# Performance work log

Hardware: AMD Instinct MI355X
Metric: run time of the kernel (lower is better)

Reference implementation:

```python
import jax, jax.numpy as jnp
import numpy as np

HEADS = 8
MAX_REL = 256
D_MODEL = 512
FFN_DIM = 2048
LN_EPS = 1e-3  # keras LayerNormalization default
NEG_INF = -1e9


def _layer_norm(x, gamma, beta):
    mu = jnp.mean(x, axis=-1, keepdims=True)
    var = jnp.var(x, axis=-1, keepdims=True)
    return (x - mu) * jax.lax.rsqrt(var + LN_EPS) * gamma + beta


def _mhra(q_in, k_in, v_in, mask, p):
    """Multi-head relative-position (Shaw-style) attention.
    mask: (B, Lq, Lk), 1.0 = masked position (added as -1e9).
    """
    B, Lq, D = q_in.shape
    Lk = k_in.shape[1]
    H = HEADS
    depth = D // H
    q = (q_in @ p['Wq'] + p['bq']).reshape(B, Lq, H, depth).transpose(0, 2, 1, 3)
    k = (k_in @ p['Wk'] + p['bk']).reshape(B, Lk, H, depth).transpose(0, 2, 1, 3)
    v = (v_in @ p['Wv'] + p['bv']).reshape(B, Lk, H, depth).transpose(0, 2, 1, 3)
    # content logits (B,H,Lq,Lk)
    logits = jnp.einsum('bhqd,bhkd->bhqk', q, k)
    # relative-position logits: project q onto clipped relative embeddings
    rel_q = jnp.einsum('bhqd,rd->bhqr', q, p['rel_emb'])  # (B,H,Lq,2K+1)
    rel_idx = jnp.clip(jnp.arange(Lk)[None, :] - jnp.arange(Lq)[:, None],
                       -MAX_REL, MAX_REL) + MAX_REL  # (Lq,Lk)
    rel_logits = jnp.take_along_axis(
        rel_q, jnp.broadcast_to(rel_idx[None, None], (B, H, Lq, Lk)), axis=-1)
    scores = (logits + rel_logits) / jnp.sqrt(jnp.asarray(depth, q.dtype))
    scores = scores + mask[:, None, :, :] * NEG_INF
    weights = jax.nn.softmax(scores, axis=-1)
    out = jnp.einsum('bhqk,bhkd->bhqd', weights, v)
    out = out.transpose(0, 2, 1, 3).reshape(B, Lq, D)
    out = out @ p['Wo'] + p['bo']
    return out, weights


def _make_attn_params(key, prefix):
    ks = jax.random.split(key, 5)
    s = 0.02
    return {
        prefix + 'Wq': jax.random.normal(ks[0], (D_MODEL, D_MODEL), jnp.float32) * s,
        prefix + 'bq': jnp.zeros((D_MODEL,), jnp.float32),
        prefix + 'Wk': jax.random.normal(ks[1], (D_MODEL, D_MODEL), jnp.float32) * s,
        prefix + 'bk': jnp.zeros((D_MODEL,), jnp.float32),
        prefix + 'Wv': jax.random.normal(ks[2], (D_MODEL, D_MODEL), jnp.float32) * s,
        prefix + 'bv': jnp.zeros((D_MODEL,), jnp.float32),
        prefix + 'Wo': jax.random.normal(ks[3], (D_MODEL, D_MODEL), jnp.float32) * s,
        prefix + 'bo': jnp.zeros((D_MODEL,), jnp.float32),
        prefix + 'rel_emb': jax.random.normal(ks[4], (2 * MAX_REL + 1, D_MODEL // HEADS), jnp.float32) * s,
        prefix + 'ln_g': jnp.ones((D_MODEL,), jnp.float32),
        prefix + 'ln_b': jnp.zeros((D_MODEL,), jnp.float32),
    }


def setup_inputs() -> dict:
    key = jax.random.key(0)
    ks = jax.random.split(key, 8)
    B, Lq, Lk = 8, 1024, 1024
    inputs = jax.random.normal(ks[0], (B, Lq, D_MODEL), jnp.float32)
    enc_kv = jax.random.normal(ks[1], (B, Lk, D_MODEL), jnp.float32)
    padding_mask = jnp.zeros((B, Lq, Lk), jnp.float32)  # no encoder padding
    causal = (jnp.arange(Lk)[None, :] > jnp.arange(Lq)[:, None]).astype(jnp.float32)
    lookahead_mask = jnp.broadcast_to(causal[None], (B, Lq, Lq)).astype(jnp.float32)
    d = {'inputs': inputs, 'enc_kv': enc_kv,
         'padding_mask': padding_mask, 'lookahead_mask': lookahead_mask,
         'training': 0}
    d.update(_make_attn_params(ks[2], 'sa_'))
    d.update(_make_attn_params(ks[3], 'ca_'))
    s = 0.02
    d['ffn_W1'] = jax.random.normal(ks[4], (D_MODEL, FFN_DIM), jnp.float32) * s
    d['ffn_b1'] = jnp.zeros((FFN_DIM,), jnp.float32)
    d['ffn_W2'] = jax.random.normal(ks[5], (FFN_DIM, D_MODEL), jnp.float32) * s
    d['ffn_b2'] = jnp.zeros((D_MODEL,), jnp.float32)
    d['ffn_ln_g'] = jnp.ones((D_MODEL,), jnp.float32)
    d['ffn_ln_b'] = jnp.zeros((D_MODEL,), jnp.float32)
    return d


def reference(inputs, enc_kv, padding_mask, lookahead_mask, training,
              sa_Wq, sa_bq, sa_Wk, sa_bk, sa_Wv, sa_bv, sa_Wo, sa_bo,
              sa_rel_emb, sa_ln_g, sa_ln_b,
              ca_Wq, ca_bq, ca_Wk, ca_bk, ca_Wv, ca_bv, ca_Wo, ca_bo,
              ca_rel_emb, ca_ln_g, ca_ln_b,
              ffn_W1, ffn_b1, ffn_W2, ffn_b2, ffn_ln_g, ffn_ln_b):
    sa = {'Wq': sa_Wq, 'bq': sa_bq, 'Wk': sa_Wk, 'bk': sa_bk,
          'Wv': sa_Wv, 'bv': sa_bv, 'Wo': sa_Wo, 'bo': sa_bo,
          'rel_emb': sa_rel_emb}
    ca = {'Wq': ca_Wq, 'bq': ca_bq, 'Wk': ca_Wk, 'bk': ca_bk,
          'Wv': ca_Wv, 'bv': ca_bv, 'Wo': ca_Wo, 'bo': ca_bo,
          'rel_emb': ca_rel_emb}
    # self attention + residual + norm (dropout identity at inference)
    attn_out, attn_w = _mhra(inputs, inputs, inputs, lookahead_mask, sa)
    attn_out = _layer_norm(inputs + attn_out, sa_ln_g, sa_ln_b)
    # cross attention + residual + norm
    ca_out, ca_w = _mhra(attn_out, enc_kv, enc_kv, padding_mask, ca)
    ca_out = _layer_norm(attn_out + ca_out, ca_ln_g, ca_ln_b)
    # pointwise FFN + residual + norm
    h = jax.nn.relu(ca_out @ ffn_W1 + ffn_b1) @ ffn_W2 + ffn_b2
    out = _layer_norm(h + ca_out, ffn_ln_g, ffn_ln_b)
    return out, attn_w, ca_w
```

## Files before the change

kernel.cpp:

```cpp
#include <hip/hip_runtime.h>
#include <hip/hip_bf16.h>
#include <cstdio>


typedef __attribute__((ext_vector_type(8))) short short8v;
typedef __attribute__((ext_vector_type(4))) short short4v;
typedef __attribute__((ext_vector_type(4))) float f32x4;

static __device__ __forceinline__ unsigned short f2bf(float f) {
    unsigned int u = __float_as_uint(f);
    unsigned int r = (u + 0x7fffu + ((u >> 16) & 1u)) >> 16;
    return (unsigned short)r;
}
static __device__ __forceinline__ float bf2f(unsigned short s) {
    return __uint_as_float(((unsigned int)s) << 16);
}

static __device__ __forceinline__ f32x4 mfma_bf16(short8v a, short8v b, f32x4 c) {
    return __builtin_amdgcn_mfma_f32_16x16x32_bf16(a, b, c, 0, 0, 0);
}

static __device__ __forceinline__ void async16(const void* g, void* l) {
    __builtin_amdgcn_global_load_lds(
        (const __attribute__((address_space(1))) unsigned int*)g,
        (__attribute__((address_space(3))) unsigned int*)l,
        16, 0, 0);
}

static __device__ __forceinline__ int swz8(int bid, int nwg) {
    return (bid & 7) * (nwg >> 3) + (bid >> 3);
}


static __device__ __forceinline__ void gemm_core(
    unsigned short* As, unsigned short* Bs,
    const unsigned short* __restrict__ A, int lda,
    const unsigned short* __restrict__ BT, int ldb,
    const float* __restrict__ bias, float* __restrict__ Cf,
    unsigned short* __restrict__ Cb, int ldc,
    int m0, int n0, int Kblk, int relu)
{
    const int t = threadIdx.x, lane = t & 63, w = t >> 6;
    const int wm = w >> 1, wn = w & 1;
    const int g = lane >> 4, l15 = lane & 15;
    f32x4 acc[4][4];
#pragma unroll
    for (int m = 0; m < 4; ++m)
#pragma unroll
        for (int n = 0; n < 4; ++n) acc[m][n] = (f32x4){0.f, 0.f, 0.f, 0.f};

    const int sgl8 = (lane & 7) ^ ((lane >> 3) & 7);
    for (int k0 = 0; k0 < Kblk; k0 += 64) {
#pragma unroll
        for (int i = 0; i < 4; ++i) {
            int rbase = w * 32 + i * 8;
            async16(A  + (size_t)(m0 + rbase + (lane >> 3)) * lda + k0 + sgl8 * 8,
                    As + rbase * 64);
            async16(BT + (size_t)(n0 + rbase + (lane >> 3)) * ldb + k0 + sgl8 * 8,
                    Bs + rbase * 64);
        }
        __syncthreads();
#pragma unroll
        for (int kk = 0; kk < 2; ++kk) {
            short8v a[4], b[4];
#pragma unroll
            for (int m = 0; m < 4; ++m) {
                int row = wm * 64 + m * 16 + l15;
                a[m] = *(const short8v*)&As[row * 64 + (((kk * 4 + g) ^ (row & 7))) * 8];
            }
#pragma unroll
            for (int n = 0; n < 4; ++n) {
                int row = wn * 64 + n * 16 + l15;
                b[n] = *(const short8v*)&Bs[row * 64 + (((kk * 4 + g) ^ (row & 7))) * 8];
            }
#pragma unroll
            for (int m = 0; m < 4; ++m)
#pragma unroll
                for (int n = 0; n < 4; ++n)
                    acc[m][n] = mfma_bf16(a[m], b[n], acc[m][n]);
        }
        __syncthreads();
    }
#pragma unroll
    for (int m = 0; m < 4; ++m) {
        int gm = m0 + wm * 64 + m * 16 + (lane >> 4) * 4;
#pragma unroll
        for (int n = 0; n < 4; ++n) {
            int gn = n0 + wn * 64 + n * 16 + (lane & 15);
            float bv = bias ? bias[gn] : 0.f;
#pragma unroll
            for (int j = 0; j < 4; ++j) {
                float v = acc[m][n][j] + bv;
                if (relu) v = fmaxf(v, 0.f);
                size_t off = (size_t)(gm + j) * ldc + gn;
                if (Cf) Cf[off] = v;
                if (Cb) Cb[off] = f2bf(v);
            }
        }
    }
}

__global__ __launch_bounds__(256) void gemm_std(
    const unsigned short* __restrict__ A, int lda,
    const unsigned short* __restrict__ BT, int ldb,
    const float* __restrict__ bias,
    float* __restrict__ Cf, unsigned short* __restrict__ Cb,
    int N, int Kblk, int relu)
{
    __shared__ __attribute__((aligned(16))) unsigned short As[128 * 64];
    __shared__ __attribute__((aligned(16))) unsigned short Bs[128 * 64];
    const int kz = blockIdx.z;
    const int nwg = gridDim.x * gridDim.y;
    const int s = swz8(blockIdx.x + gridDim.x * blockIdx.y, nwg);
    const int bx = s % gridDim.x, by = s / gridDim.x;
    const size_t part = (size_t)kz * gridDim.y * 128 * N;
    gemm_core(As, Bs, A + kz * Kblk, lda, BT + kz * Kblk, ldb,
              kz == 0 ? bias : nullptr,
              Cf ? Cf + part : nullptr, Cb, N,
              by * 128, bx * 128, Kblk, relu);
}

__global__ __launch_bounds__(256) void gemm_ca(
    const unsigned short* __restrict__ Ekv, const unsigned short* __restrict__ Xq,
    const unsigned short* __restrict__ WkvT, const unsigned short* __restrict__ WqT,
    const float* __restrict__ bkv, const float* __restrict__ bq,
    unsigned short* __restrict__ KV, unsigned short* __restrict__ Q)
{
    __shared__ __attribute__((aligned(16))) unsigned short As[128 * 64];
    __shared__ __attribute__((aligned(16))) unsigned short Bs[128 * 64];
    const int nwg = gridDim.x * gridDim.y;
    const int s = swz8(blockIdx.x + gridDim.x * blockIdx.y, nwg);
    const int bx = s % gridDim.x, by = s / gridDim.x;
    if (bx < 8)
        gemm_core(As, Bs, Ekv, 512, WkvT, 512, bkv, nullptr, KV, 1024,
                  by * 128, bx * 128, 512, 0);
    else
        gemm_core(As, Bs, Xq, 512, WqT, 512, bq, nullptr, Q, 512,
                  by * 128, (bx - 8) * 128, 512, 0);
}

__global__ __launch_bounds__(256, 3) void fused_attn(
    const unsigned short* __restrict__ Qp, int qstride,
    const unsigned short* __restrict__ Kp, int kstride,
    const unsigned short* __restrict__ Vt,
    const unsigned short* __restrict__ relW,
    const unsigned short* __restrict__ maskb,
    float* __restrict__ Wout,
    unsigned short* __restrict__ Hout)
{
    __shared__ __attribute__((aligned(16))) unsigned short Qs[16 * 64];
    __shared__ __attribute__((aligned(16))) unsigned short U[24576];
    __shared__ float Red[2][4][16];
    unsigned short* Ks  = U;
    unsigned short* Rel = U;
    unsigned short* Pl  = U;
    unsigned short* Vs  = U + 16384;
    const int t = threadIdx.x, lane = t & 63, w = t >> 6;
    const int g = lane >> 4, l15 = lane & 15;
    const int s = swz8(blockIdx.x + gridDim.x * blockIdx.y, 4096);
    const int bh = s >> 6, b = bh >> 3, h = bh & 7;
    const int q0 = (s & 63) * 16;
    const int sgl8 = (lane & 7) ^ ((lane >> 3) & 7);

    if (w < 2) {
        int row = w * 8 + (lane >> 3);
        async16(Qp + (size_t)(b * 1024 + q0 + row) * qstride + h * 64 + sgl8 * 8,
                &Qs[w * 512]);
    }
    __syncthreads();

    short8v qa[2];
#pragma unroll
    for (int kk = 0; kk < 2; ++kk)
        qa[kk] = *(const short8v*)&Qs[l15 * 64 + (((kk * 4 + g) ^ (l15 & 7))) * 8];

    f32x4 acc[16];
#pragma unroll
    for (int i = 0; i < 16; ++i) acc[i] = (f32x4){0.f, 0.f, 0.f, 0.f};

#pragma unroll
    for (int qtr = 0; qtr < 4; ++qtr) {
#pragma unroll
        for (int c = 0; c < 8; ++c) {
            int rbase = w * 64 + c * 8;
            async16(Kp + (size_t)(b * 1024 + qtr * 256 + rbase + (lane >> 3)) * kstride
                       + h * 64 + sgl8 * 8,
                    &Ks[rbase * 64]);
        }
        __syncthreads();
#pragma unroll
        for (int n = 0; n < 4; ++n) {
            int row = w * 64 + n * 16 + l15;
            short8v kb0 = *(const short8v*)&Ks[row * 64 + ((g ^ (row & 7))) * 8];
            short8v kb1 = *(const short8v*)&Ks[row * 64 + (((4 + g) ^ (row & 7))) * 8];
            acc[qtr * 4 + n] = mfma_bf16(qa[0], kb0, acc[qtr * 4 + n]);
            acc[qtr * 4 + n] = mfma_bf16(qa[1], kb1, acc[qtr * 4 + n]);
        }
        __syncthreads();
    }

    for (int rs = w; rs < 33; rs += 4) {
        int rc = rs * 16 + l15;
        int re = rc > 512 ? 512 : rc;
        short8v b0 = *(const short8v*)(relW + (size_t)re * 64 + g * 8);
        short8v b1 = *(const short8v*)(relW + (size_t)re * 64 + 32 + g * 8);
        f32x4 r4 = (f32x4){0.f, 0.f, 0.f, 0.f};
        r4 = mfma_bf16(qa[0], b0, r4);
        r4 = mfma_bf16(qa[1], b1, r4);
#pragma unroll
        for (int j = 0; j < 4; ++j)
            Rel[(g * 4 + j) * 528 + rs * 16 + l15] = f2bf(r4[j]);
    }
    __syncthreads();

    const int qb = q0 + g * 4;
    const int ql = g * 4;
    const unsigned short* mrow = maskb + ((size_t)b * 1024 + qb) * 1024;
#pragma unroll
    for (int na = 0; na < 16; ++na) {
        int k = (na >> 2) * 256 + w * 64 + (na & 3) * 16 + l15;
#pragma unroll
        for (int j = 0; j < 4; ++j) {
            int q = qb + j;
            int d = k - q; d = d < -256 ? -256 : (d > 256 ? 256 : d);
            float rel = bf2f(Rel[(ql + j) * 528 + d + 256]);
            float mv = bf2f(mrow[(size_t)j * 1024 + k]);
            acc[na][j] = (acc[na][j] + rel) * 0.125f + mv;
        }
    }

    float mx[4];
#pragma unroll
    for (int j = 0; j < 4; ++j) {
        float m = acc[0][j];
#pragma unroll
        for (int na = 1; na < 16; ++na) m = fmaxf(m, acc[na][j]);
#pragma unroll
        for (int off = 1; off < 16; off <<= 1) m = fmaxf(m, __shfl_xor(m, off));
        mx[j] = m;
    }
    if (l15 == 0) {
#pragma unroll
        for (int j = 0; j < 4; ++j) Red[0][w][ql + j] = mx[j];
    }
    __syncthreads();
#pragma unroll
    for (int j = 0; j < 4; ++j) {
        float m = Red[0][0][ql + j];
        m = fmaxf(m, Red[0][1][ql + j]);
        m = fmaxf(m, Red[0][2][ql + j]);
        m = fmaxf(m, Red[0][3][ql + j]);
        mx[j] = m;
    }

    float sm[4] = {0.f, 0.f, 0.f, 0.f};
#pragma unroll
    for (int na = 0; na < 16; ++na)
#pragma unroll
        for (int j = 0; j < 4; ++j) {
            float e = __expf(acc[na][j] - mx[j]);
            acc[na][j] = e;
            sm[j] += e;
        }
#pragma unroll
    for (int j = 0; j < 4; ++j)
#pragma unroll
        for (int off = 1; off < 16; off <<= 1) sm[j] += __shfl_xor(sm[j], off);
    if (l15 == 0) {
#pragma unroll
        for (int j = 0; j < 4; ++j) Red[1][w][ql + j] = sm[j];
    }
    __syncthreads();
#pragma unroll
    for (int j = 0; j < 4; ++j) {
        float ssum = Red[1][0][ql + j] + Red[1][1][ql + j]
                   + Red[1][2][ql + j] + Red[1][3][ql + j];
        sm[j] = 1.0f / ssum;
    }

    float* wbase = Wout + ((size_t)bh * 1024 + qb) * 1024;
#pragma unroll
    for (int na = 0; na < 16; ++na) {
        int k = (na >> 2) * 256 + w * 64 + (na & 3) * 16 + l15;
#pragma unroll
        for (int j = 0; j < 4; ++j) {
            float p = acc[na][j] * sm[j];
            __builtin_nontemporal_store(p, &wbase[(size_t)j * 1024 + k]);
            Pl[((k >> 3) * 16 + (ql + j)) * 8 + (k & 7)] = f2bf(p);
        }
    }
    __syncthreads();

    f32x4 oacc = (f32x4){0.f, 0.f, 0.f, 0.f};
#pragma unroll
    for (int c = 0; c < 8; ++c) {
        {
            int idx = w * 4;
#pragma unroll
            for (int i = 0; i < 4; ++i) {
                int d = (idx + i) * 4 + (lane >> 4);
                int gl = (lane & 15) ^ (d & 15);
                async16(Vt + ((size_t)bh * 64 + d) * 1024 + c * 128 + gl * 8,
                        &Vs[(idx + i) * 512]);
            }
        }
        __syncthreads();
#pragma unroll
        for (int ks = 0; ks < 4; ++ks) {
            int kg = c * 4 + ks;
            short8v a = *(const short8v*)&Pl[((kg * 4 + g) * 16 + l15) * 8];
            int rowv = w * 16 + l15;
            short8v bb = *(const short8v*)&Vs[rowv * 128 + (((ks * 4 + g) ^ (rowv & 15))) * 8];
            oacc = mfma_bf16(a, bb, oacc);
        }
        __syncthreads();
    }
#pragma unroll
    for (int j = 0; j < 4; ++j)
        Hout[(size_t)(b * 1024 + q0 + g * 4 + j) * 512 + h * 64 + w * 16 + l15]
            = f2bf(oacc[j]);
}

__global__ __launch_bounds__(256) void transpose_v(
    const unsigned short* __restrict__ Vb, int stride, unsigned short* __restrict__ Vt)
{
    __shared__ unsigned short T[128][72];
    const int bh = blockIdx.y, b = bh >> 3, h = bh & 7;
    const int k0 = blockIdx.x * 128;
    const int t = threadIdx.x;
    {
        int r = t >> 1, half = t & 1;
        const unsigned short* gp = Vb + (size_t)(b * 1024 + k0 + r) * stride + h * 64 + half * 32;
#pragma unroll
        for (int i = 0; i < 8; ++i)
            *(short4v*)&T[r][half * 32 + i * 4] = *(const short4v*)(gp + i * 4);
    }
    __syncthreads();
    {
        int d = t >> 2, qtr = t & 3;
        unsigned short* gp = Vt + ((size_t)bh * 64 + d) * 1024 + k0 + qtr * 32;
#pragma unroll
        for (int i = 0; i < 32; i += 4) {
            short4v v;
            v.x = T[qtr * 32 + i + 0][d];
            v.y = T[qtr * 32 + i + 1][d];
            v.z = T[qtr * 32 + i + 2][d];
            v.w = T[qtr * 32 + i + 3][d];
            *(short4v*)(gp + i) = v;
        }
    }
}

__global__ __launch_bounds__(128) void ln512(
    const float* __restrict__ Xp0, const float* __restrict__ Xp1,
    const float* __restrict__ Res,
    const float* __restrict__ g, const float* __restrict__ be,
    float* __restrict__ out, unsigned short* __restrict__ outb)
{
    const size_t row = blockIdx.x;
    const int t = threadIdx.x;
    float4 x = *(const float4*)(Xp0 + row * 512 + t * 4);
    float4 r = *(const float4*)(Res + row * 512 + t * 4);
    x.x += r.x; x.y += r.y; x.z += r.z; x.w += r.w;
    if (Xp1) {
        float4 p = *(const float4*)(Xp1 + row * 512 + t * 4);
        x.x += p.x; x.y += p.y; x.z += p.z; x.w += p.w;
    }
    float s  = x.x + x.y + x.z + x.w;
    float ss = x.x * x.x + x.y * x.y + x.z * x.z + x.w * x.w;
#pragma unroll
    for (int o = 32; o > 0; o >>= 1) { s += __shfl_xor(s, o); ss += __shfl_xor(ss, o); }
    __shared__ float sm[2], sq[2];
    if ((t & 63) == 0) { sm[t >> 6] = s; sq[t >> 6] = ss; }
    __syncthreads();
    s = sm[0] + sm[1]; ss = sq[0] + sq[1];
    const float mean = s * (1.f / 512.f);
    const float var  = ss * (1.f / 512.f) - mean * mean;
    const float rstd = rsqrtf(var + 1e-3f);
    float4 gv = *(const float4*)(g + t * 4), bv = *(const float4*)(be + t * 4);
    float4 o;
    o.x = (x.x - mean) * rstd * gv.x + bv.x;
    o.y = (x.y - mean) * rstd * gv.y + bv.y;
    o.z = (x.z - mean) * rstd * gv.z + bv.z;
    o.w = (x.w - mean) * rstd * gv.w + bv.w;
    *(float4*)(out + row * 512 + t * 4) = o;
    if (outb) {
        short4v q4;
        q4.x = f2bf(o.x); q4.y = f2bf(o.y); q4.z = f2bf(o.z); q4.w = f2bf(o.w);
        *(short4v*)(outb + row * 512 + t * 4) = q4;
    }
}

static __device__ __forceinline__ void wt_tile(
    const float* __restrict__ W, unsigned short* __restrict__ WT,
    int K, int N, int k0, int n0)
{
    __shared__ float T[64][68];
    const int t = threadIdx.x;
    int r = t >> 4, c = (t & 15) * 4;
#pragma unroll
    for (int p = 0; p < 4; ++p) {
        float4 v = *(const float4*)(W + (size_t)(k0 + r + p * 16) * N + n0 + c);
        T[r + p * 16][c + 0] = v.x; T[r + p * 16][c + 1] = v.y;
        T[r + p * 16][c + 2] = v.z; T[r + p * 16][c + 3] = v.w;
    }
    __syncthreads();
#pragma unroll
    for (int p = 0; p < 4; ++p) {
        int n = r + p * 16;
        short4v o;
        o.x = f2bf(T[c + 0][n]); o.y = f2bf(T[c + 1][n]);
        o.z = f2bf(T[c + 2][n]); o.w = f2bf(T[c + 3][n]);
        *(short4v*)(WT + (size_t)(n0 + n) * K + k0 + c) = o;
    }
}

__global__ __launch_bounds__(256) void wt_cast(
    const float* __restrict__ W, unsigned short* __restrict__ WT, int K, int N)
{
    wt_tile(W, WT, K, N, blockIdx.y * 64, blockIdx.x * 64);
}

struct Ptr8 {
    const float* s[8];
    unsigned short* d[8];
};

__global__ __launch_bounds__(256) void wt_cast8(Ptr8 p)
{
    wt_tile(p.s[blockIdx.z], p.d[blockIdx.z], 512, 512,
            blockIdx.y * 64, blockIdx.x * 64);
}

__global__ __launch_bounds__(256) void misc_prep(
    const float* __restrict__ sarel, const float* __restrict__ carel,
    unsigned short* __restrict__ relSA, unsigned short* __restrict__ relCA,
    const float* __restrict__ sabq, const float* __restrict__ sabk,
    const float* __restrict__ sabv, float* __restrict__ bqkv,
    const float* __restrict__ cabk, const float* __restrict__ cabv,
    float* __restrict__ bkv)
{
    const int bid = blockIdx.x, t = threadIdx.x;
    if (bid < 33) {
        int i = bid * 256 + t;
        if (i < 8208) {
            float4 v = *(const float4*)(sarel + (size_t)i * 4);
            short4v s;
            s.x = f2bf(v.x); s.y = f2bf(v.y); s.z = f2bf(v.z); s.w = f2bf(v.w);
            *(short4v*)(relSA + (size_t)i * 4) = s;
        }
    } else if (bid < 66) {
        int i = (bid - 33) * 256 + t;
        if (i < 8208) {
            float4 v = *(const float4*)(carel + (size_t)i * 4);
            short4v s;
            s.x = f2bf(v.x); s.y = f2bf(v.y); s.z = f2bf(v.z); s.w = f2bf(v.w);
            *(short4v*)(relCA + (size_t)i * 4) = s;
        }
    } else if (bid == 66) {
        for (int i = t; i < 1536; i += 256)
            bqkv[i] = i < 512 ? sabq[i] : (i < 1024 ? sabk[i - 512] : sabv[i - 1024]);
    } else {
        for (int i = t; i < 1024; i += 256)
            bkv[i] = i < 512 ? cabk[i] : cabv[i - 512];
    }
}

__global__ __launch_bounds__(256) void cast_all(
    const float* __restrict__ a, unsigned short* __restrict__ oa,
    const float* __restrict__ b, unsigned short* __restrict__ ob,
    const float* __restrict__ m0, unsigned short* __restrict__ om0,
    const float* __restrict__ m1, unsigned short* __restrict__ om1)
{
    size_t i = (size_t)blockIdx.x * 256 + threadIdx.x;
    const float* src; unsigned short* dst; float scale;
    if (i < 1048576)      { src = a;  dst = oa;  scale = 1.f; }
    else if (i < 2097152) { src = b;  dst = ob;  scale = 1.f; i -= 1048576; }
    else if (i < 4194304) { src = m0; dst = om0; scale = -1e9f; i -= 2097152; }
    else                  { src = m1; dst = om1; scale = -1e9f; i -= 4194304; }
    const float4* sp = (const float4*)(src + i * 4);
    float4 v;
    v.x = __builtin_nontemporal_load(&((const float*)sp)[0]);
    v.y = __builtin_nontemporal_load(&((const float*)sp)[1]);
    v.z = __builtin_nontemporal_load(&((const float*)sp)[2]);
    v.w = __builtin_nontemporal_load(&((const float*)sp)[3]);
    short4v s;
    s.x = f2bf(v.x * scale); s.y = f2bf(v.y * scale);
    s.z = f2bf(v.z * scale); s.w = f2bf(v.w * scale);
    *(short4v*)(dst + i * 4) = s;
}


extern "C" void kernel_launch(void* const* d_in, const int* in_sizes, int n_in,
                              void* d_out, int out_size, void* d_ws, size_t ws_size,
                              hipStream_t stream)
{
    (void)in_sizes; (void)n_in; (void)out_size;
    const float* inputs    = (const float*)d_in[0];
    const float* enc_kv    = (const float*)d_in[1];
    const float* pad_mask  = (const float*)d_in[2];
    const float* look_mask = (const float*)d_in[3];
    const float* saWq  = (const float*)d_in[5];
    const float* sabq  = (const float*)d_in[6];
    const float* saWk  = (const float*)d_in[7];
    const float* sabk  = (const float*)d_in[8];
    const float* saWv  = (const float*)d_in[9];
    const float* sabv  = (const float*)d_in[10];
    const float* saWo  = (const float*)d_in[11];
    const float* sabo  = (const float*)d_in[12];
    const float* sarel = (const float*)d_in[13];
    const float* salg  = (const float*)d_in[14];
    const float* salb  = (const float*)d_in[15];
    const float* caWq  = (const float*)d_in[16];
    const float* cabq  = (const float*)d_in[17];
    const float* caWk  = (const float*)d_in[18];
    const float* cabk  = (const float*)d_in[19];
    const float* caWv  = (const float*)d_in[20];
    const float* cabv  = (const float*)d_in[21];
    const float* caWo  = (const float*)d_in[22];
    const float* cabo  = (const float*)d_in[23];
    const float* carel = (const float*)d_in[24];
    const float* calg  = (const float*)d_in[25];
    const float* calb  = (const float*)d_in[26];
    const float* fW1   = (const float*)d_in[27];
    const float* fb1   = (const float*)d_in[28];
    const float* fW2   = (const float*)d_in[29];
    const float* fb2   = (const float*)d_in[30];
    const float* flg   = (const float*)d_in[31];
    const float* flb   = (const float*)d_in[32];

    float* out    = (float*)d_out;
    float* attn_w = out + (size_t)8 * 1024 * 512;
    float* ca_w   = attn_w + (size_t)8 * 8 * 1024 * 1024;

    char* ws = (char*)d_ws;
    size_t off = 0;
    unsigned short* WTa = (unsigned short*)(ws + off); off += 8519936;
    float* bqkv = (float*)(ws + off); off += 8192;
    float* bkv  = (float*)(ws + off); off += 8192;
    unsigned short* Abf   = (unsigned short*)(ws + off); off += 8388608;
    unsigned short* Ebf   = (unsigned short*)(ws + off); off += 8388608;
    unsigned short* x1bf  = (unsigned short*)(ws + off); off += 8388608;
    unsigned short* Qca   = (unsigned short*)(ws + off); off += 8388608;
    unsigned short* heads = (unsigned short*)(ws + off); off += 8388608;
    unsigned short* Vt    = (unsigned short*)(ws + off); off += 8388608;
    unsigned short* mskSA = (unsigned short*)(ws + off); off += 16777216;
    unsigned short* mskCA = (unsigned short*)(ws + off); off += 16777216;
    unsigned short* KV    = (unsigned short*)(ws + off); off += 16777216;
    unsigned short* big   = (unsigned short*)(ws + off); off += 33554432;
    float* x1 = (float*)(ws + off); off += 16777216;
    float* x2 = (float*)(ws + off); off += 16777216;
    float* Pb = (float*)(ws + off); off += 33554432;
    if (ws_size < off) {
        fprintf(stderr, "kernel_launch: ws too small (%zu < %zu)\n", ws_size, off);
        return;
    }
    float* Pb1 = Pb + 4194304;
    unsigned short* QKV    = big;
    unsigned short* hidden = big;
    unsigned short* x2bf   = Abf;

    unsigned short* saWqT = WTa + 0;
    unsigned short* saWkT = WTa + 262144;
    unsigned short* saWvT = WTa + 524288;
    unsigned short* saWoT = WTa + 786432;
    unsigned short* caWqT = WTa + 1048576;
    unsigned short* caWkT = WTa + 1310720;
    unsigned short* caWvT = WTa + 1572864;
    unsigned short* caWoT = WTa + 1835008;
    unsigned short* W1T   = WTa + 2097152;
    unsigned short* W2T   = WTa + 3145728;
    unsigned short* relSA = WTa + 4194304;
    unsigned short* relCA = WTa + 4227136;

    const dim3 T256(256), T128(128);

    Ptr8 p8;
    p8.s[0] = saWq; p8.d[0] = saWqT;
    p8.s[1] = saWk; p8.d[1] = saWkT;
    p8.s[2] = saWv; p8.d[2] = saWvT;
    p8.s[3] = saWo; p8.d[3] = saWoT;
    p8.s[4] = caWq; p8.d[4] = caWqT;
    p8.s[5] = caWk; p8.d[5] = caWkT;
    p8.s[6] = caWv; p8.d[6] = caWvT;
    p8.s[7] = caWo; p8.d[7] = caWoT;
    wt_cast8<<<dim3(8, 8, 8), T256, 0, stream>>>(p8);
    wt_cast<<<dim3(32, 8), T256, 0, stream>>>(fW1, W1T, 512, 2048);
    wt_cast<<<dim3(8, 32), T256, 0, stream>>>(fW2, W2T, 2048, 512);
    misc_prep<<<dim3(68), T256, 0, stream>>>(sarel, carel, relSA, relCA,
                                             sabq, sabk, sabv, bqkv, cabk, cabv, bkv);
    cast_all<<<dim3(24576), T256, 0, stream>>>(inputs, Abf, enc_kv, Ebf,
                                               look_mask, mskSA, pad_mask, mskCA);

    gemm_std<<<dim3(12, 64, 1), T256, 0, stream>>>(Abf, 512, WTa, 512, bqkv,
                                                   nullptr, QKV, 1536, 512, 0);
    transpose_v<<<dim3(8, 64), T256, 0, stream>>>(QKV + 1024, 1536, Vt);
    fused_attn<<<dim3(64, 64), T256, 0, stream>>>(QKV, 1536, QKV + 512, 1536, Vt,
                                                  relSA, mskSA, attn_w, heads);
    gemm_std<<<dim3(4, 64, 2), T256, 0, stream>>>(heads, 512, saWoT, 512, sabo,
                                                  Pb, nullptr, 512, 256, 0);
    ln512<<<dim3(8192), T128, 0, stream>>>(Pb, Pb1, inputs, salg, salb, x1, x1bf);

    gemm_ca<<<dim3(12, 64), T256, 0, stream>>>(Ebf, x1bf, caWkT, caWqT,
                                               bkv, cabq, KV, Qca);
    transpose_v<<<dim3(8, 64), T256, 0, stream>>>(KV + 512, 1024, Vt);
    fused_attn<<<dim3(64, 64), T256, 0, stream>>>(Qca, 512, KV, 1024, Vt,
                                                  relCA, mskCA, ca_w, heads);
    gemm_std<<<dim3(4, 64, 2), T256, 0, stream>>>(heads, 512, caWoT, 512, cabo,
                                                  Pb, nullptr, 512, 256, 0);
    ln512<<<dim3(8192), T128, 0, stream>>>(Pb, Pb1, x1, calg, calb, x2, x2bf);

    gemm_std<<<dim3(16, 64, 1), T256, 0, stream>>>(x2bf, 512, W1T, 512, fb1,
                                                   nullptr, hidden, 2048, 512, 1);
    gemm_std<<<dim3(4, 64, 2), T256, 0, stream>>>(hidden, 2048, W2T, 2048, fb2,
                                                  Pb, nullptr, 512, 1024, 0);
    ln512<<<dim3(8192), T128, 0, stream>>>(Pb, Pb1, x2, flg, flb, out, nullptr);
}
```

Before: 494.1 us.

## Overlap relative-logit MFMA with K tile loads; merge weight-cast launches

The relative-position projection tiles are now computed inside the K-loading loop, while the async K loads for each quarter are in flight. The results go into a separate LDS region beside the K buffer, with the clipped-at-512 column held in a small extra array. This removes a serial phase and one barrier from the attention kernel, at the cost of a branch on every rel lookup. Separately, the three weight transpose/cast kernels are merged into one launch to cut launch overhead.

After: 493.3 us. Within noise of the previous version (-0.2%).

```diff
diff --git a/kernel.cpp b/kernel.cpp
--- a/kernel.cpp
+++ b/kernel.cpp
@@ -151,10 +151,11 @@
     __shared__ __attribute__((aligned(16))) unsigned short Qs[16 * 64];
     __shared__ __attribute__((aligned(16))) unsigned short U[24576];
     __shared__ float Red[2][4][16];
-    unsigned short* Ks  = U;
-    unsigned short* Rel = U;
-    unsigned short* Pl  = U;
-    unsigned short* Vs  = U + 16384;
+    __shared__ unsigned short R512[16];
+    unsigned short* Ks   = U;
+    unsigned short* Pl   = U;
+    unsigned short* RelV = U + 16384;
+    unsigned short* Vs   = U + 16384;
     const int t = threadIdx.x, lane = t & 63, w = t >> 6;
     const int g = lane >> 4, l15 = lane & 15;
     const int s = swz8(blockIdx.x + gridDim.x * blockIdx.y, 4096);
@@ -174,32 +175,7 @@
     for (int kk = 0; kk < 2; ++kk)
         qa[kk] = *(const short8v*)&Qs[l15 * 64 + (((kk * 4 + g) ^ (l15 & 7))) * 8];
 
-    f32x4 acc[16];
-#pragma unroll
-    for (int i = 0; i < 16; ++i) acc[i] = (f32x4){0.f, 0.f, 0.f, 0.f};
-
-#pragma unroll
-    for (int qtr = 0; qtr < 4; ++qtr) {
-#pragma unroll
-        for (int c = 0; c < 8; ++c) {
-            int rbase = w * 64 + c * 8;
-            async16(Kp + (size_t)(b * 1024 + qtr * 256 + rbase + (lane >> 3)) * kstride
-                       + h * 64 + sgl8 * 8,
-                    &Ks[rbase * 64]);
-        }
-        __syncthreads();
-#pragma unroll
-        for (int n = 0; n < 4; ++n) {
-            int row = w * 64 + n * 16 + l15;
-            short8v kb0 = *(const short8v*)&Ks[row * 64 + ((g ^ (row & 7))) * 8];
-            short8v kb1 = *(const short8v*)&Ks[row * 64 + (((4 + g) ^ (row & 7))) * 8];
-            acc[qtr * 4 + n] = mfma_bf16(qa[0], kb0, acc[qtr * 4 + n]);
-            acc[qtr * 4 + n] = mfma_bf16(qa[1], kb1, acc[qtr * 4 + n]);
-        }
-        __syncthreads();
-    }
-
-    for (int rs = w; rs < 33; rs += 4) {
+    auto relTile = [&](int rs) {
         int rc = rs * 16 + l15;
         int re = rc > 512 ? 512 : rc;
         short8v b0 = *(const short8v*)(relW + (size_t)re * 64 + g * 8);
@@ -207,11 +183,44 @@
         f32x4 r4 = (f32x4){0.f, 0.f, 0.f, 0.f};
         r4 = mfma_bf16(qa[0], b0, r4);
         r4 = mfma_bf16(qa[1], b1, r4);
-#pragma unroll
-        for (int j = 0; j < 4; ++j)
-            Rel[(g * 4 + j) * 528 + rs * 16 + l15] = f2bf(r4[j]);
-    }
-    __syncthreads();
+        if (rs < 32) {
+#pragma unroll
+            for (int j = 0; j < 4; ++j)
+                RelV[(g * 4 + j) * 512 + rs * 16 + l15] = f2bf(r4[j]);
+        } else if (l15 == 0) {
+#pragma unroll
+            for (int j = 0; j < 4; ++j)
+                R512[g * 4 + j] = f2bf(r4[j]);
+        }
+    };
+
+    f32x4 acc[16];
+#pragma unroll
+    for (int i = 0; i < 16; ++i) acc[i] = (f32x4){0.f, 0.f, 0.f, 0.f};
+
+#pragma unroll
+    for (int qtr = 0; qtr < 4; ++qtr) {
+#pragma unroll
+        for (int c = 0; c < 8; ++c) {
+            int rbase = w * 64 + c * 8;
+            async16(Kp + (size_t)(b * 1024 + qtr * 256 + rbase + (lane >> 3)) * kstride
+                       + h * 64 + sgl8 * 8,
+                    &Ks[rbase * 64]);
+        }
+        relTile(8 * qtr + w);
+        relTile(8 * qtr + w + 4);
+        if (qtr == 3 && w == 0) relTile(32);
+        __syncthreads();
+#pragma unroll
+        for (int n = 0; n < 4; ++n) {
+            int row = w * 64 + n * 16 + l15;
+            short8v kb0 = *(const short8v*)&Ks[row * 64 + ((g ^ (row & 7))) * 8];
+            short8v kb1 = *(const short8v*)&Ks[row * 64 + (((4 + g) ^ (row & 7))) * 8];
+            acc[qtr * 4 + n] = mfma_bf16(qa[0], kb0, acc[qtr * 4 + n]);
+            acc[qtr * 4 + n] = mfma_bf16(qa[1], kb1, acc[qtr * 4 + n]);
+        }
+        __syncthreads();
+    }
 
     const int qb = q0 + g * 4;
     const int ql = g * 4;
@@ -223,7 +232,9 @@
         for (int j = 0; j < 4; ++j) {
             int q = qb + j;
             int d = k - q; d = d < -256 ? -256 : (d > 256 ? 256 : d);
-            float rel = bf2f(Rel[(ql + j) * 528 + d + 256]);
+            int idx = d + 256;
+            float rel = (idx < 512) ? bf2f(RelV[(ql + j) * 512 + idx])
+                                    : bf2f(R512[ql + j]);
             float mv = bf2f(mrow[(size_t)j * 1024 + k]);
             acc[na][j] = (acc[na][j] + rel) * 0.125f + mv;
         }
@@ -415,21 +426,26 @@
     }
 }
 
-__global__ __launch_bounds__(256) void wt_cast(
-    const float* __restrict__ W, unsigned short* __restrict__ WT, int K, int N)
-{
-    wt_tile(W, WT, K, N, blockIdx.y * 64, blockIdx.x * 64);
-}
-
 struct Ptr8 {
     const float* s[8];
     unsigned short* d[8];
 };
 
-__global__ __launch_bounds__(256) void wt_cast8(Ptr8 p)
-{
-    wt_tile(p.s[blockIdx.z], p.d[blockIdx.z], 512, 512,
-            blockIdx.y * 64, blockIdx.x * 64);
+__global__ __launch_bounds__(256) void wt_cast_all(
+    Ptr8 p, const float* __restrict__ fW1, unsigned short* __restrict__ W1T,
+    const float* __restrict__ fW2, unsigned short* __restrict__ W2T)
+{
+    const int bid = blockIdx.x;
+    if (bid < 512) {
+        int mat = bid >> 6, tile = bid & 63;
+        wt_tile(p.s[mat], p.d[mat], 512, 512, (tile >> 3) * 64, (tile & 7) * 64);
+    } else if (bid < 768) {
+        int tile = bid - 512;
+        wt_tile(fW1, W1T, 512, 2048, (tile >> 5) * 64, (tile & 31) * 64);
+    } else {
+        int tile = bid - 768;
+        wt_tile(fW2, W2T, 2048, 512, (tile >> 3) * 64, (tile & 7) * 64);
+    }
 }
 
 __global__ __launch_bounds__(256) void misc_prep(
@@ -584,9 +600,7 @@
     p8.s[5] = caWk; p8.d[5] = caWkT;
     p8.s[6] = caWv; p8.d[6] = caWvT;
     p8.s[7] = caWo; p8.d[7] = caWoT;
-    wt_cast8<<<dim3(8, 8, 8), T256, 0, stream>>>(p8);
-    wt_cast<<<dim3(32, 8), T256, 0, stream>>>(fW1, W1T, 512, 2048);
-    wt_cast<<<dim3(8, 32), T256, 0, stream>>>(fW2, W2T, 2048, 512);
+    wt_cast_all<<<dim3(1024), T256, 0, stream>>>(p8, fW1, W1T, fW2, W2T);
     misc_prep<<<dim3(68), T256, 0, stream>>>(sarel, carel, relSA, relCA,
                                              sabq, sabk, sabv, bqkv, cabk, cabv, bkv);
     cast_all<<<dim3(24576), T256, 0, stream>>>(inputs, Abf, enc_kv, Ebf,
```
